# Optimization experiments

Hardware: AMD Instinct MI355X
Metric: run time of the kernel (lower is better)

## Reference

```python
import jax, jax.numpy as jnp
import numpy as np

LEAF = 32
N = 262144          # num_nodes, power of 2
NLEV = 8            # HODLR levels
RANK = 16           # off-diagonal low-rank
NNZ = 1310720       # ~5 nnz per row


def setup_inputs() -> dict:
    key = jax.random.key(0)
    ks = jax.random.split(key, 24)
    inp = {}
    inp["leaf_blocks"] = jax.random.normal(ks[0], (1, N // LEAF, LEAF, LEAF), jnp.float32) * 0.1
    for l in range(NLEV):
        inp[f"u{l}"] = jax.random.normal(ks[1 + 2 * l], (1, N, RANK), jnp.float32) * 0.05
        inp[f"v{l}"] = jax.random.normal(ks[2 + 2 * l], (1, N, RANK), jnp.float32) * 0.05
    inp["A_indices"] = jax.random.randint(ks[17], (2, NNZ), 0, N, dtype=jnp.int32).astype(jnp.int64)
    inp["A_values"] = jax.random.normal(ks[18], (NNZ,), jnp.float32)
    inp["z"] = jax.random.normal(ks[19], (1, N, 1), jnp.float32)
    inp["num_nodes"] = N
    return inp


def apply_hodlr(leaf_blocks, factors, x, leaf_size=LEAF):
    # x: [B, n, 1]; leaf_blocks: [B, n/leaf, leaf, leaf]
    B, n, _ = x.shape
    nb = n // leaf_size
    xb = x.reshape(B, nb, leaf_size, 1)
    L = leaf_blocks
    # y = L @ (L^T @ x) + 1e-4 * x  per leaf block
    yb = jnp.matmul(L, jnp.matmul(jnp.swapaxes(L, -1, -2), xb)) + xb * 1e-4
    y = yb.reshape(B, n, 1)
    for li, (u, v) in enumerate(factors):
        num_splits = 2 ** (li + 1)
        bs = n // num_splits
        if bs == 0:
            continue
        npair = num_splits // 2
        vl = npair * 2 * bs  # == n for power-of-2 n
        xv = x[:, :vl].reshape(B, npair, 2, bs, 1)
        uv = u[:, :vl].reshape(B, npair, 2, bs, -1)
        vv = v[:, :vl].reshape(B, npair, 2, bs, -1)
        xL, xR = xv[:, :, 0], xv[:, :, 1]
        uL, uR = uv[:, :, 0], uv[:, :, 1]
        vL, vR = vv[:, :, 0], vv[:, :, 1]
        # cross-block low-rank updates: y_L += U_L (V_R^T x_R), y_R += U_R (V_L^T x_L)
        yL = jnp.matmul(uL, jnp.matmul(jnp.swapaxes(vR, -1, -2), xR))
        yR = jnp.matmul(uR, jnp.matmul(jnp.swapaxes(vL, -1, -2), xL))
        upd = jnp.stack([yL, yR], axis=2).reshape(B, vl, 1)
        if vl < n:
            upd = jnp.pad(upd, ((0, 0), (0, n - vl), (0, 0)))
        y = y + upd
    return y


def reference(leaf_blocks, u0, v0, u1, v1, u2, v2, u3, v3, u4, v4, u5, v5, u6, v6, u7, v7,
              A_indices, A_values, z, num_nodes):
    factors = [(u0, v0), (u1, v1), (u2, v2), (u3, v3),
               (u4, v4), (u5, v5), (u6, v6), (u7, v7)]
    w = apply_hodlr(leaf_blocks, factors, z)           # [1, N, 1]
    w_flat = w[0, :, 0]                                 # [N]
    rows, cols = A_indices[0], A_indices[1]
    # sparse COO matvec: y[r] = sum_k A_values[k] * w[cols[k]] over rows
    y_flat = jax.ops.segment_sum(A_values * w_flat[cols], rows, num_segments=num_nodes)
    y = y_flat.reshape(1, num_nodes, 1)
    return jnp.mean((y - z) ** 2)
```

## Files before the change

kernel.cpp:

```cpp
#include <hip/hip_runtime.h>

#define NN 262144
#define RANK 16
#define NNZ_K 1310720

struct P8 { const float* p[8]; };

__global__ __launch_bounds__(256) void k_levels_t(P8 v, const float* __restrict__ z,
                                                  float* __restrict__ part) {
    __shared__ float zl[512];
    __shared__ float red[8][4][16];
    const int tid  = threadIdx.x;
    const int base = blockIdx.x * 512;

    zl[tid]       = z[base + tid];
    zl[tid + 256] = z[base + tid + 256];
    __syncthreads();

    const int q = tid & 3;
    const int e = tid >> 2;

    float4 acc[8];
#pragma unroll
    for (int l = 0; l < 8; ++l) acc[l] = make_float4(0.f, 0.f, 0.f, 0.f);

#pragma unroll
    for (int it = 0; it < 8; ++it) {
        const int jloc = it * 64 + e;
        const size_t j = (size_t)(base + jloc);
        const float zz = zl[jloc];
#pragma unroll
        for (int l = 0; l < 8; ++l) {
            const float4 vv = *(const float4*)(v.p[l] + j * RANK + q * 4);
            acc[l].x += vv.x * zz;
            acc[l].y += vv.y * zz;
            acc[l].z += vv.z * zz;
            acc[l].w += vv.w * zz;
        }
    }

    const int lane = tid & 63;
    const int wv   = tid >> 6;
#pragma unroll
    for (int l = 0; l < 8; ++l) {
        float4 a = acc[l];
#pragma unroll
        for (int m = 4; m <= 32; m <<= 1) {
            a.x += __shfl_xor(a.x, m);
            a.y += __shfl_xor(a.y, m);
            a.z += __shfl_xor(a.z, m);
            a.w += __shfl_xor(a.w, m);
        }
        if (lane < 4) *(float4*)&red[l][wv][lane * 4] = a;
    }
    __syncthreads();

    if (tid < 128) {
        const int l = tid >> 4;
        const int r = tid & 15;
        const float s = red[l][0][r] + red[l][1][r] + red[l][2][r] + red[l][3][r];
        part[(l * 512 + blockIdx.x) * 16 + r] = s;
    }
}

__global__ __launch_bounds__(64) void k_reduce_t(const float* __restrict__ part,
                                                 float* __restrict__ tg,
                                                 float* __restrict__ loss) {
    const int b = blockIdx.x;
    if (b == 0 && threadIdx.x == 0) loss[0] = 0.f;
    const int t = b + 2;
    const int l = 30 - __clz(t);
    const int h = t - (2 << l);
    const int cnt = 256 >> l;
    const int c0  = h * cnt;
    const int r = threadIdx.x & 15;
    const int g = threadIdx.x >> 4;

    float s = 0.f;
    for (int c = c0 + g; c < c0 + cnt; c += 4)
        s += part[(l * 512 + c) * 16 + r];

    __shared__ float red[64];
    red[threadIdx.x] = s;
    __syncthreads();
    if (threadIdx.x < 16)
        tg[((2 << l) - 2 + h) * 16 + r] = red[r] + red[16 + r] + red[32 + r] + red[48 + r];
}

__global__ __launch_bounds__(256) void k_apply(const float* __restrict__ leaf, P8 u,
                                               const float* __restrict__ z,
                                               const float* __restrict__ tg,
                                               float* __restrict__ w,
                                               float* __restrict__ y) {
    __shared__ float Lp[8 * 1056];
    __shared__ float xl[256];
    __shared__ float t32[8][32];
    __shared__ float tl[8][16];

    const int tid  = threadIdx.x;
    const int base = blockIdx.x * 256;

    const float4* Lg = (const float4*)(leaf + (size_t)base * 32);
#pragma unroll
    for (int k = 0; k < 8; ++k) {
        const int fi = tid + k * 256;
        const float4 val = Lg[fi];
        const int lb  = fi >> 8;
        const int off = (fi & 255) * 4;
        const int row = off >> 5;
        const int col = off & 31;
        float* d = &Lp[lb * 1056 + row * 33 + col];
        d[0] = val.x; d[1] = val.y; d[2] = val.z; d[3] = val.w;
    }
    xl[tid] = z[base + tid];
    if (tid < 128) {
        const int l = tid >> 4;
        const int r = tid & 15;
        const int h = base >> (17 - l);
        tl[l][r] = tg[(((2 << l) - 2) + (h ^ 1)) * 16 + r];
    }
    __syncthreads();

    {
        const int lb = tid >> 5;
        const int c  = tid & 31;
        const float* Lb = &Lp[lb * 1056];
        const float* xb = &xl[lb * 32];
        float s = 0.f;
#pragma unroll
        for (int row = 0; row < 32; ++row)
            s += Lb[row * 33 + c] * xb[row];
        t32[lb][c] = s;
    }
    __syncthreads();

    {
        const int lb = tid >> 5;
        const int r  = tid & 31;
        const float* Lb = &Lp[lb * 1056 + r * 33];
        float acc = 1e-4f * xl[tid];
#pragma unroll
        for (int c = 0; c < 32; ++c)
            acc += Lb[c] * t32[lb][c];

        const size_t i = (size_t)(base + tid);
#pragma unroll
        for (int l = 0; l < 8; ++l) {
            const float4* up = (const float4*)(u.p[l] + i * RANK);
            const float4 a0 = up[0], a1 = up[1], a2 = up[2], a3 = up[3];
            acc += a0.x * tl[l][0]  + a0.y * tl[l][1]  + a0.z * tl[l][2]  + a0.w * tl[l][3]
                 + a1.x * tl[l][4]  + a1.y * tl[l][5]  + a1.z * tl[l][6]  + a1.w * tl[l][7]
                 + a2.x * tl[l][8]  + a2.y * tl[l][9]  + a2.z * tl[l][10] + a2.w * tl[l][11]
                 + a3.x * tl[l][12] + a3.y * tl[l][13] + a3.z * tl[l][14] + a3.w * tl[l][15];
        }
        w[i] = acc;
        y[i] = 0.f;
    }
}

__global__ __launch_bounds__(256) void k_spmv(const int* __restrict__ idx,
                                              const float* __restrict__ vals,
                                              const float* __restrict__ w,
                                              float* __restrict__ y) {
    const int k = (blockIdx.x * 256 + threadIdx.x) * 4;
    const int4   r4 = *(const int4*)(idx + k);
    const int4   c4 = *(const int4*)(idx + NNZ_K + k);
    const float4 v4 = *(const float4*)(vals + k);
    atomicAdd(&y[r4.x], v4.x * w[c4.x]);
    atomicAdd(&y[r4.y], v4.y * w[c4.y]);
    atomicAdd(&y[r4.z], v4.z * w[c4.z]);
    atomicAdd(&y[r4.w], v4.w * w[c4.w]);
}

__global__ __launch_bounds__(256) void k_loss(const float* __restrict__ y,
                                              const float* __restrict__ z,
                                              float* __restrict__ loss) {
    const int i = blockIdx.x * 256 + threadIdx.x;
    const float4 a = ((const float4*)y)[i];
    const float4 b = ((const float4*)z)[i];
    const float dx = a.x - b.x, dy = a.y - b.y, dz = a.z - b.z, dw = a.w - b.w;
    float s = dx * dx + dy * dy + dz * dz + dw * dw;
#pragma unroll
    for (int m = 32; m >= 1; m >>= 1) s += __shfl_down(s, m);
    __shared__ float r4[4];
    const int lane = threadIdx.x & 63, wv = threadIdx.x >> 6;
    if (lane == 0) r4[wv] = s;
    __syncthreads();
    if (threadIdx.x == 0) atomicAdd(loss, r4[0] + r4[1] + r4[2] + r4[3]);
}

__global__ void k_fin(const float* __restrict__ loss, float* __restrict__ out) {
    out[0] = loss[0] * (1.0f / (float)NN);
}

extern "C" void kernel_launch(void* const* d_in, const int* in_sizes, int n_in,
                              void* d_out, int out_size, void* d_ws, size_t ws_size,
                              hipStream_t stream) {
    const float* leaf = (const float*)d_in[0];
    P8 u, v;
    for (int l = 0; l < 8; ++l) {
        u.p[l] = (const float*)d_in[1 + 2 * l];
        v.p[l] = (const float*)d_in[2 + 2 * l];
    }
    const int*   Aidx  = (const int*)d_in[17];
    const float* Avals = (const float*)d_in[18];
    const float* z     = (const float*)d_in[19];

    float* ws   = (float*)d_ws;
    float* part = ws;
    float* tg   = ws + 65536;
    float* loss = ws + 73728;
    float* y    = ws + 81920;
    float* w    = ws + 81920 + NN;

    k_levels_t<<<NN / 512, 256, 0, stream>>>(v, z, part);
    k_reduce_t<<<510, 64, 0, stream>>>(part, tg, loss);
    k_apply  <<<NN / 256, 256, 0, stream>>>(leaf, u, z, tg, w, y);
    k_spmv   <<<NNZ_K / 1024, 256, 0, stream>>>(Aidx, Avals, w, y);
    k_loss   <<<NN / 1024, 256, 0, stream>>>(y, z, loss);
    k_fin    <<<1, 1, 0, stream>>>(loss, (float*)d_out);
}
```

Before: 401.8 us.

## Replace global-atomic COO SpMV with row-bucket binning and LDS accumulation

The scatter SpMV, which did one global atomicAdd per nonzero, is replaced by two passes. First, each block computes its products and counting-sorts them into 256 row buckets in shared memory, writing (value,row) pairs plus per-bucket offsets to workspace. Second, one block per bucket accumulates its 1024 rows with LDS atomics and computes the squared-error loss in the same kernel, so the y buffer and the separate loss kernel are no longer needed. This trades random global atomics for about 10 MB of extra pair traffic, and the per-thread serial segment loops read memory poorly coalesced. The new path only runs when the workspace is large enough; otherwise the old path is used.

```diff
diff --git a/kernel.cpp b/kernel.cpp
--- a/kernel.cpp
+++ b/kernel.cpp
@@ -3,6 +3,10 @@
 #define NN 262144
 #define RANK 16
 #define NNZ_K 1310720
+#define NB 640
+#define BPB 2048
+#define NBKT 256
+#define RPB 1024
 
 struct P8 { const float* p[8]; };
 
@@ -154,7 +158,115 @@
                  + a3.x * tl[l][12] + a3.y * tl[l][13] + a3.z * tl[l][14] + a3.w * tl[l][15];
         }
         w[i] = acc;
-        y[i] = 0.f;
+        if (y) y[i] = 0.f;
+    }
+}
+
+__global__ __launch_bounds__(256) void k_bin(const int* __restrict__ idx,
+                                             const float* __restrict__ vals,
+                                             const float* __restrict__ w,
+                                             unsigned long long* __restrict__ gpairs,
+                                             int* __restrict__ gdesc) {
+    __shared__ unsigned long long pairs[BPB];
+    __shared__ int hist[NBKT];
+    __shared__ int scan[NBKT];
+    __shared__ int cursor[NBKT];
+
+    const int t  = threadIdx.x;
+    const int bl = blockIdx.x;
+    const int base = bl * BPB;
+
+    hist[t] = 0;
+    __syncthreads();
+
+    int   rows[8];
+    float pv[8];
+#pragma unroll
+    for (int i = 0; i < 2; ++i) {
+        const int k = base + i * 1024 + t * 4;
+        const int4   r4 = *(const int4*)(idx + k);
+        const int4   c4 = *(const int4*)(idx + NNZ_K + k);
+        const float4 v4 = *(const float4*)(vals + k);
+        rows[i*4+0] = r4.x; pv[i*4+0] = v4.x * w[c4.x];
+        rows[i*4+1] = r4.y; pv[i*4+1] = v4.y * w[c4.y];
+        rows[i*4+2] = r4.z; pv[i*4+2] = v4.z * w[c4.z];
+        rows[i*4+3] = r4.w; pv[i*4+3] = v4.w * w[c4.w];
+        atomicAdd(&hist[r4.x >> 10], 1);
+        atomicAdd(&hist[r4.y >> 10], 1);
+        atomicAdd(&hist[r4.z >> 10], 1);
+        atomicAdd(&hist[r4.w >> 10], 1);
+    }
+    __syncthreads();
+
+    const int cnt = hist[t];
+    scan[t] = cnt;
+    __syncthreads();
+    for (int off = 1; off < NBKT; off <<= 1) {
+        const int add = (t >= off) ? scan[t - off] : 0;
+        __syncthreads();
+        scan[t] += add;
+        __syncthreads();
+    }
+    const int st = scan[t] - cnt;
+    gdesc[t * NB + bl] = st | (cnt << 16);
+    cursor[t] = st;
+    __syncthreads();
+
+#pragma unroll
+    for (int i = 0; i < 8; ++i) {
+        const int b   = rows[i] >> 10;
+        const int pos = atomicAdd(&cursor[b], 1);
+        pairs[pos] = ((unsigned long long)__float_as_uint(pv[i]) << 32) | (unsigned)rows[i];
+    }
+    __syncthreads();
+
+    const ulonglong2* ps = (const ulonglong2*)pairs;
+    ulonglong2*       pd = (ulonglong2*)(gpairs + (size_t)bl * BPB);
+#pragma unroll
+    for (int i = 0; i < 4; ++i)
+        pd[i * 256 + t] = ps[i * 256 + t];
+}
+
+__global__ __launch_bounds__(512) void k_accum(const unsigned long long* __restrict__ gpairs,
+                                               const int* __restrict__ gdesc,
+                                               const float* __restrict__ z,
+                                               float* __restrict__ loss) {
+    __shared__ float acc[RPB];
+    __shared__ float red[8];
+    const int t = threadIdx.x;
+    const int b = blockIdx.x;
+    acc[t] = 0.f;
+    acc[t + 512] = 0.f;
+    __syncthreads();
+
+    for (int bl = t; bl < NB; bl += 512) {
+        const int d  = gdesc[b * NB + bl];
+        const int st = d & 0xffff;
+        const int c  = d >> 16;
+        const unsigned long long* p = gpairs + (size_t)bl * BPB + st;
+        for (int j = 0; j < c; ++j) {
+            const unsigned long long pr = p[j];
+            atomicAdd(&acc[(int)(pr & 1023u)], __uint_as_float((unsigned)(pr >> 32)));
+        }
+    }
+    __syncthreads();
+
+    float s = 0.f;
+#pragma unroll
+    for (int i = 0; i < 2; ++i) {
+        const int r = i * 512 + t;
+        const float d = acc[r] - z[b * RPB + r];
+        s += d * d;
+    }
+#pragma unroll
+    for (int m = 32; m >= 1; m >>= 1) s += __shfl_down(s, m);
+    if ((t & 63) == 0) red[t >> 6] = s;
+    __syncthreads();
+    if (t == 0) {
+        float tt = 0.f;
+#pragma unroll
+        for (int i = 0; i < 8; ++i) tt += red[i];
+        atomicAdd(loss, tt);
     }
 }
 
@@ -182,11 +294,11 @@
     float s = dx * dx + dy * dy + dz * dz + dw * dw;
 #pragma unroll
     for (int m = 32; m >= 1; m >>= 1) s += __shfl_down(s, m);
-    __shared__ float r4[4];
+    __shared__ float r4s[4];
     const int lane = threadIdx.x & 63, wv = threadIdx.x >> 6;
-    if (lane == 0) r4[wv] = s;
-    __syncthreads();
-    if (threadIdx.x == 0) atomicAdd(loss, r4[0] + r4[1] + r4[2] + r4[3]);
+    if (lane == 0) r4s[wv] = s;
+    __syncthreads();
+    if (threadIdx.x == 0) atomicAdd(loss, r4s[0] + r4s[1] + r4s[2] + r4s[3]);
 }
 
 __global__ void k_fin(const float* __restrict__ loss, float* __restrict__ out) {
@@ -207,16 +319,26 @@
     const float* z     = (const float*)d_in[19];
 
     float* ws   = (float*)d_ws;
-    float* part = ws;
-    float* tg   = ws + 65536;
-    float* loss = ws + 73728;
-    float* y    = ws + 81920;
-    float* w    = ws + 81920 + NN;
+    float* part  = ws;
+    float* tg    = ws + 65536;
+    float* loss  = ws + 73728;
+    float* w     = ws + 73792;
+    int*   gdesc = (int*)(ws + 335936);
+    unsigned long long* gpairs = (unsigned long long*)(ws + 499776);
+    const size_t need_main = (size_t)(499776 + (size_t)NB * BPB * 2) * 4;
 
     k_levels_t<<<NN / 512, 256, 0, stream>>>(v, z, part);
     k_reduce_t<<<510, 64, 0, stream>>>(part, tg, loss);
-    k_apply  <<<NN / 256, 256, 0, stream>>>(leaf, u, z, tg, w, y);
-    k_spmv   <<<NNZ_K / 1024, 256, 0, stream>>>(Aidx, Avals, w, y);
-    k_loss   <<<NN / 1024, 256, 0, stream>>>(y, z, loss);
-    k_fin    <<<1, 1, 0, stream>>>(loss, (float*)d_out);
-}
+
+    if (ws_size >= need_main) {
+        k_apply<<<NN / 256, 256, 0, stream>>>(leaf, u, z, tg, w, nullptr);
+        k_bin  <<<NB, 256, 0, stream>>>(Aidx, Avals, w, gpairs, gdesc);
+        k_accum<<<NBKT, 512, 0, stream>>>(gpairs, gdesc, z, loss);
+    } else {
+        float* y = ws + 335936;
+        k_apply<<<NN / 256, 256, 0, stream>>>(leaf, u, z, tg, w, y);
+        k_spmv <<<NNZ_K / 1024, 256, 0, stream>>>(Aidx, Avals, w, y);
+        k_loss <<<NN / 1024, 256, 0, stream>>>(y, z, loss);
+    }
+    k_fin<<<1, 1, 0, stream>>>(loss, (float*)d_out);
+}
```

Result: faster. 353.7 us (-12.0%).
